# Kernel optimization log

Hardware: AMD Instinct MI355X
Metric: run time of the kernel (lower is better)

## Reference

```python
import jax, jax.numpy as jnp
import numpy as np
from itertools import product

C0, C1, C_IN, C_OUT = 16, 32, 1, 32
GRID = 768

def _enc(c):
    # injective int64 hash of 3D integer coords (values in [-4, 2043])
    return ((c[:, 0] + 4) * 2048 + (c[:, 1] + 4)) * 2048 + (c[:, 2] + 4)

def _build_km(coords, offsets):
    # kernel map for a stride-1 conv on one coordinate set:
    # per kernel offset o, pairs (in_idx, out_idx) with coords[in] == coords[out] + o
    N = coords.shape[0]
    keys = _enc(coords)
    order = np.argsort(keys)
    skeys = keys[order]
    ins, outs = [], []
    for o in offsets:
        qk = _enc(coords + np.asarray(o, np.int64))
        pos = np.searchsorted(skeys, qk)
        posc = np.clip(pos, 0, N - 1)
        valid = skeys[posc] == qk
        ins.append(order[posc[valid]].astype(np.int32))
        outs.append(np.nonzero(valid)[0].astype(np.int32))
    P = max(len(a) for a in ins)
    km_in = np.full((len(offsets), P), N, np.int32)   # pad -> zero row of x
    km_out = np.full((len(offsets), P), N, np.int32)  # pad -> dropped out row
    for k in range(len(offsets)):
        km_in[k, :len(ins[k])] = ins[k]
        km_out[k, :len(outs[k])] = outs[k]
    return km_in, km_out

def setup_inputs() -> dict:
    # voxelized surface heightfield: realistic sparse 3D point cloud occupancy
    xs, ys = np.meshgrid(np.arange(GRID), np.arange(GRID), indexing='ij')
    z = np.round(40.0 * np.sin(xs / 24.0) + 40.0 * np.cos(ys / 24.0)).astype(np.int64) + 128
    coords0 = np.stack([xs.ravel(), ys.ravel(), z.ravel()], 1).astype(np.int64)
    n0 = coords0.shape[0]
    offs27 = list(product((-1, 0, 1), repeat=3))
    km0_in, km0_out = _build_km(coords0, offs27)

    # stride-2 kernel-2 downsample: out coord = floor(c/2), offset = c mod 2
    u2 = coords0 // 2
    coords1, inv = np.unique(u2, axis=0, return_inverse=True)
    inv = inv.reshape(-1)
    n1 = coords1.shape[0]
    o = coords0 - 2 * u2
    kk = o[:, 0] * 4 + o[:, 1] * 2 + o[:, 2]
    ins, outs = [], []
    for k in range(8):
        m = np.nonzero(kk == k)[0]
        ins.append(m.astype(np.int32))
        outs.append(inv[m].astype(np.int32))
    P = max(len(a) for a in ins)
    kmd_in = np.full((8, P), n0, np.int32)
    kmd_out = np.full((8, P), n1, np.int32)
    for k in range(8):
        kmd_in[k, :len(ins[k])] = ins[k]
        kmd_out[k, :len(outs[k])] = outs[k]

    km1_in, km1_out = _build_km(coords1, offs27)

    key = jax.random.key(0)
    ks = jax.random.split(key, 6)
    w = lambda k, sh: jax.random.normal(k, sh, jnp.float32) * 0.1
    z32 = lambda c: jnp.zeros((c,), jnp.float32)
    return dict(
        in_feats=jnp.ones((n0, C_IN), jnp.float32),
        W_first=w(ks[0], (27, C_IN, C0)), b_first=z32(C0),
        W_pre=w(ks[1], (27, C0, C0)), b_pre=z32(C0),
        W_down=w(ks[2], (8, C0, C1)), b_down=z32(C1),
        W_r0=w(ks[3], (27, C1, C1)), b_r0=z32(C1),
        W_r1=w(ks[4], (27, C1, C1)), b_r1=z32(C1),
        W_fin=w(ks[5], (27, C1, C_OUT)), b_fin=z32(C_OUT),
        km0_in=jnp.asarray(km0_in), km0_out=jnp.asarray(km0_out),
        kmd_in=jnp.asarray(kmd_in), kmd_out=jnp.asarray(kmd_out),
        km1_in=jnp.asarray(km1_in), km1_out=jnp.asarray(km1_out),
        n1=int(n1),
    )

def _sparse_conv(x, W, b, km_in, km_out, n_out):
    # gather-GEMM-scatter sparse conv: out[j] += x[i] @ W[k] over pairs of offset k
    xp = jnp.concatenate([x, jnp.zeros((1, x.shape[1]), x.dtype)], 0)
    out = jnp.zeros((n_out + 1, W.shape[-1]), x.dtype)
    for k in range(W.shape[0]):  # static small loop over kernel offsets
        out = out.at[km_out[k]].add(xp[km_in[k]] @ W[k])
    return out[:n_out] + b

def reference(in_feats, W_first, b_first, W_pre, b_pre, W_down, b_down,
              W_r0, b_r0, W_r1, b_r1, W_fin, b_fin,
              km0_in, km0_out, kmd_in, kmd_out, km1_in, km1_out, n1):
    n0 = in_feats.shape[0]
    relu = jax.nn.relu
    # first_block: 3^3 conv + relu
    x = relu(_sparse_conv(in_feats, W_first, b_first, km0_in, km0_out, n0))
    cached = x  # cached_feature_list[0] (use_skip_connection=False)
    # blocks[0]: conv3x3 + relu, stride-2 downsample conv + relu
    x = relu(_sparse_conv(x, W_pre, b_pre, km0_in, km0_out, n0))
    x = relu(_sparse_conv(x, W_down, b_down, kmd_in, kmd_out, n1))
    # ResBlock
    r = relu(_sparse_conv(x, W_r0, b_r0, km1_in, km1_out, n1))
    r = _sparse_conv(r, W_r1, b_r1, km1_in, km1_out, n1)
    x = r + x
    # final conv (act=None)
    out = _sparse_conv(x, W_fin, b_fin, km1_in, km1_out, n1)
    return (out, cached)
```

## Files before the change

### kernel.cpp

```cpp
#include <hip/hip_runtime.h>


#define TPB 256
#define TPC 128

typedef __attribute__((ext_vector_type(8))) short short8;
typedef __attribute__((ext_vector_type(4))) float floatx4;

static __device__ __forceinline__ unsigned short f2b(float f) {
    union { float f; unsigned u; } v; v.f = f;
    unsigned r = v.u + 0x7fffu + ((v.u >> 16) & 1u);
    return (unsigned short)(r >> 16);
}
static __device__ __forceinline__ float b2f(unsigned short h) {
    union { unsigned u; float f; } v; v.u = ((unsigned)h) << 16;
    return v.f;
}

__global__ void scatter_tab(const int* __restrict__ km_in,
                            const int* __restrict__ km_out,
                            int* __restrict__ tab, long long rowcap, long long P,
                            long long total) {
    long long t = (long long)blockIdx.x * blockDim.x + threadIdx.x;
    if (t >= total) return;
    long long k = t / P;
    int o = km_out[t];
    tab[k * rowcap + o] = km_in[t];
}

__global__ void zero_pads(unsigned short* a, unsigned short* b, unsigned short* c,
                          unsigned short* d, unsigned short* e) {
    int t = threadIdx.x;
    if (t < 16) a[t] = 0;
    else if (t < 32) b[t - 16] = 0;
    else if (t < 64) c[t - 32] = 0;
    else if (t < 96) d[t - 64] = 0;
    else if (t < 128) e[t - 96] = 0;
}

__global__ void pack_w32(const float* __restrict__ W, unsigned short* __restrict__ Wp,
                         int K) {
    int t = blockIdx.x * blockDim.x + threadIdx.x;
    if (t >= K * 1024) return;
    int j = t & 7, n = (t >> 3) & 31, q = (t >> 8) & 3, k = t >> 10;
    Wp[t] = f2b(W[(k * 32 + q * 8 + j) * 32 + n]);
}

__global__ void pack_w16(const float* __restrict__ W, unsigned short* __restrict__ Wp,
                         int K2, int COUT, int Ksrc) {
    int t = blockIdx.x * blockDim.x + threadIdx.x;
    if (t >= K2 * 4 * COUT * 8) return;
    int j = t & 7;
    int r = t >> 3;
    int n = r % COUT; r /= COUT;
    int q = r & 3;
    int k2 = r >> 2;
    int ks = 2 * k2 + (q >> 1);
    int cin = (q & 1) * 8 + j;
    float v = (ks < Ksrc) ? W[(ks * 16 + cin) * COUT + n] : 0.f;
    Wp[t] = f2b(v);
}

__global__ __launch_bounds__(TPB) void conv_first_k(
    const float* __restrict__ xin, const float* __restrict__ W,
    const float* __restrict__ b, const int* __restrict__ tab, long long rowcap,
    int n0, float* __restrict__ outf, unsigned short* __restrict__ outb) {
    int j = blockIdx.x * blockDim.x + threadIdx.x;
    if (j >= n0) return;
    float acc[16];
#pragma unroll
    for (int c = 0; c < 16; ++c) acc[c] = b[c];
#pragma unroll
    for (int k = 0; k < 27; ++k) {
        int idx = tab[(long long)k * rowcap + j];
        bool ok = (unsigned)idx < (unsigned)n0;
        int cidx = ok ? idx : 0;
        float v = xin[cidx];
        v = ok ? v : 0.f;
        const float* Wk = W + k * 16;
#pragma unroll
        for (int c = 0; c < 16; ++c) acc[c] = fmaf(v, Wk[c], acc[c]);
    }
    float* orow = outf + (long long)j * 16;
    unsigned short* brow = outb + (long long)j * 16;
#pragma unroll
    for (int c = 0; c < 16; ++c) {
        float v = fmaxf(acc[c], 0.f);
        orow[c] = v;
        brow[c] = f2b(v);
    }
}

template <int CIN, int COUT, int STEPS, bool RELU, bool RES, bool WF32, bool WB16>
__global__ __launch_bounds__(TPC, 6) void conv_mfma(
    const unsigned short* __restrict__ xb,
    const unsigned short* __restrict__ Wp,
    const float* __restrict__ bias,
    const int* __restrict__ tab, long long rowcap, int n_in, int n_out,
    const unsigned short* __restrict__ resb,
    float* __restrict__ outf, unsigned short* __restrict__ outb) {
    constexpr int NT = COUT / 16;
    constexpr int CP = COUT + 4;
    __shared__ float red[64][CP];
    int w = (int)threadIdx.x >> 6;
    int lane = (int)threadIdx.x & 63;
    int m = lane & 15, q = lane >> 4;
    long long j0 = (long long)blockIdx.x * 64;

    floatx4 acc[4][NT];
#pragma unroll
    for (int t = 0; t < 4; ++t)
#pragma unroll
        for (int nt = 0; nt < NT; ++nt) acc[t][nt] = floatx4{0.f, 0.f, 0.f, 0.f};

    const int coff = (CIN == 32) ? q * 8 : (q & 1) * 8;
    constexpr int HSTEPS = (STEPS + 1) / 2;
#pragma unroll
    for (int i = 0; i < HSTEPS; ++i) {
        int s = 2 * i + w;
        if (s >= STEPS) break;
        int ks = (CIN == 32) ? s : 2 * s + (q >> 1);
        const int* trow = tab + (long long)ks * rowcap + j0 + m;
        int idx[4];
#pragma unroll
        for (int t = 0; t < 4; ++t) {
            unsigned v = (unsigned)trow[16 * t];
            idx[t] = (int)(v < (unsigned)n_in ? v : (unsigned)n_in);
        }
        short8 b0 = *(const short8*)(Wp + (((s * 4 + q) * COUT) + m) * 8);
        short8 b1;
        if (NT == 2) b1 = *(const short8*)(Wp + (((s * 4 + q) * COUT) + 16 + m) * 8);
#pragma unroll
        for (int t = 0; t < 4; ++t) {
            short8 a = *(const short8*)(xb + (long long)idx[t] * CIN + coff);
            acc[t][0] = __builtin_amdgcn_mfma_f32_16x16x32_bf16(a, b0, acc[t][0], 0, 0, 0);
            if (NT == 2)
                acc[t][1] = __builtin_amdgcn_mfma_f32_16x16x32_bf16(a, b1, acc[t][1], 0, 0, 0);
        }
    }

    if (w == 1) {
#pragma unroll
        for (int t = 0; t < 4; ++t)
#pragma unroll
            for (int u = 0; u < 4; ++u)
#pragma unroll
                for (int nt = 0; nt < NT; ++nt)
                    red[16 * t + 4 * q + u][16 * nt + m] = acc[t][nt][u];
    }
    __syncthreads();
    if (w == 1) return;

    float bs[2];
    bs[0] = bias[m];
    if (NT == 2) bs[1] = bias[16 + m];
#pragma unroll
    for (int t = 0; t < 4; ++t) {
#pragma unroll
        for (int u = 0; u < 4; ++u) {
            long long r = j0 + 16 * t + q * 4 + u;
            if (r < n_out) {
#pragma unroll
                for (int nt = 0; nt < NT; ++nt) {
                    float v = acc[t][nt][u] + red[16 * t + 4 * q + u][16 * nt + m] + bs[nt];
                    if (RES) v += b2f(resb[r * COUT + nt * 16 + m]);
                    if (RELU) v = fmaxf(v, 0.f);
                    if (WF32) outf[r * COUT + nt * 16 + m] = v;
                    if (WB16) outb[r * COUT + nt * 16 + m] = f2b(v);
                }
            }
        }
    }
}

static inline unsigned nblk(long long n, int b) { return (unsigned)((n + b - 1) / b); }
static inline size_t align64(size_t x) { return (x + 63) & ~(size_t)63; }

extern "C" void kernel_launch(void* const* d_in, const int* in_sizes, int n_in_cnt,
                              void* d_out, int out_size, void* d_ws, size_t ws_size,
                              hipStream_t stream) {
    const float* in_feats = (const float*)d_in[0];
    const float* W_first = (const float*)d_in[1];
    const float* b_first = (const float*)d_in[2];
    const float* W_pre   = (const float*)d_in[3];
    const float* b_pre   = (const float*)d_in[4];
    const float* W_down  = (const float*)d_in[5];
    const float* b_down  = (const float*)d_in[6];
    const float* W_r0    = (const float*)d_in[7];
    const float* b_r0    = (const float*)d_in[8];
    const float* W_r1    = (const float*)d_in[9];
    const float* b_r1    = (const float*)d_in[10];
    const float* W_fin   = (const float*)d_in[11];
    const float* b_fin   = (const float*)d_in[12];
    const int* km0_in  = (const int*)d_in[13];
    const int* km0_out = (const int*)d_in[14];
    const int* kmd_in  = (const int*)d_in[15];
    const int* kmd_out = (const int*)d_in[16];
    const int* km1_in  = (const int*)d_in[17];
    const int* km1_out = (const int*)d_in[18];

    const int n0 = in_sizes[0];
    const int n1 = (out_size - 16 * n0) / 32;
    const long long P0 = in_sizes[13] / 27;
    const long long Pd = in_sizes[15] / 8;
    const long long P1 = in_sizes[17] / 27;

    const long long rc0 = ((n0 + 64) / 64) * 64;
    const long long rc1 = ((n1 + 64) / 64) * 64;

    float* out_lo = (float*)d_out;
    float* cached = out_lo + (size_t)n1 * 32;

    char* base = (char*)d_ws;
    size_t off = 0;
    auto alloc = [&](size_t bytes) { void* p = base + off; off = align64(off + bytes); return p; };
    int* t0 = (int*)alloc(sizeof(int) * 28 * rc0);
    int* t1 = (int*)alloc(sizeof(int) * 27 * rc1);
    int* td = (int*)alloc(sizeof(int) * 8 * rc1);
    unsigned short* c0b   = (unsigned short*)alloc(sizeof(short) * 16 * (n0 + 1));
    unsigned short* x0pre = (unsigned short*)alloc(sizeof(short) * 16 * (n0 + 1));
    unsigned short* x1a   = (unsigned short*)alloc(sizeof(short) * 32 * (n1 + 1));
    unsigned short* x1b   = (unsigned short*)alloc(sizeof(short) * 32 * (n1 + 1));
    unsigned short* x1c   = (unsigned short*)alloc(sizeof(short) * 32 * (n1 + 1));
    unsigned short* wp_pre  = (unsigned short*)alloc(sizeof(short) * 14 * 4 * 16 * 8);
    unsigned short* wp_down = (unsigned short*)alloc(sizeof(short) * 4 * 4 * 32 * 8);
    unsigned short* wp_r0   = (unsigned short*)alloc(sizeof(short) * 27 * 1024);
    unsigned short* wp_r1   = (unsigned short*)alloc(sizeof(short) * 27 * 1024);
    unsigned short* wp_fin  = (unsigned short*)alloc(sizeof(short) * 27 * 1024);
    (void)ws_size; (void)n_in_cnt;

    scatter_tab<<<nblk(27 * P0, TPB), TPB, 0, stream>>>(km0_in, km0_out, t0, rc0, P0, 27 * P0);
    scatter_tab<<<nblk(27 * P1, TPB), TPB, 0, stream>>>(km1_in, km1_out, t1, rc1, P1, 27 * P1);
    scatter_tab<<<nblk(8 * Pd, TPB), TPB, 0, stream>>>(kmd_in, kmd_out, td, rc1, Pd, 8 * Pd);

    pack_w16<<<nblk(14 * 4 * 16 * 8, TPB), TPB, 0, stream>>>(W_pre, wp_pre, 14, 16, 27);
    pack_w16<<<nblk(4 * 4 * 32 * 8, TPB), TPB, 0, stream>>>(W_down, wp_down, 4, 32, 8);
    pack_w32<<<nblk(27 * 1024, TPB), TPB, 0, stream>>>(W_r0, wp_r0, 27);
    pack_w32<<<nblk(27 * 1024, TPB), TPB, 0, stream>>>(W_r1, wp_r1, 27);
    pack_w32<<<nblk(27 * 1024, TPB), TPB, 0, stream>>>(W_fin, wp_fin, 27);
    zero_pads<<<1, 160, 0, stream>>>(c0b + (size_t)n0 * 16, x0pre + (size_t)n0 * 16,
                                     x1a + (size_t)n1 * 32, x1b + (size_t)n1 * 32,
                                     x1c + (size_t)n1 * 32);

    conv_first_k<<<nblk(n0, TPB), TPB, 0, stream>>>(in_feats, W_first, b_first, t0, rc0,
                                                    n0, cached, c0b);
    const unsigned g0 = nblk(n0, 64), g1 = nblk(n1, 64);
    conv_mfma<16, 16, 14, true, false, false, true><<<g0, TPC, 0, stream>>>(
        c0b, wp_pre, b_pre, t0, rc0, n0, n0, nullptr, nullptr, x0pre);
    conv_mfma<16, 32, 4, true, false, false, true><<<g1, TPC, 0, stream>>>(
        x0pre, wp_down, b_down, td, rc1, n0, n1, nullptr, nullptr, x1a);
    conv_mfma<32, 32, 27, true, false, false, true><<<g1, TPC, 0, stream>>>(
        x1a, wp_r0, b_r0, t1, rc1, n1, n1, nullptr, nullptr, x1b);
    conv_mfma<32, 32, 27, false, true, false, true><<<g1, TPC, 0, stream>>>(
        x1b, wp_r1, b_r1, t1, rc1, n1, n1, x1a, nullptr, x1c);
    conv_mfma<32, 32, 27, false, false, true, false><<<g1, TPC, 0, stream>>>(
        x1c, wp_fin, b_fin, t1, rc1, n1, n1, nullptr, out_lo, nullptr);
}
```

Before: 527.7 us.

## Assign one 64-row tile per wave, drop LDS split-K reduction, fuse pack kernels

```diff
diff --git a/kernel.cpp b/kernel.cpp
--- a/kernel.cpp
+++ b/kernel.cpp
@@ -2,7 +2,6 @@
 
 
 #define TPB 256
-#define TPC 128
 
 typedef __attribute__((ext_vector_type(8))) short short8;
 typedef __attribute__((ext_vector_type(4))) float floatx4;
@@ -28,28 +27,9 @@
     tab[k * rowcap + o] = km_in[t];
 }
 
-__global__ void zero_pads(unsigned short* a, unsigned short* b, unsigned short* c,
-                          unsigned short* d, unsigned short* e) {
-    int t = threadIdx.x;
-    if (t < 16) a[t] = 0;
-    else if (t < 32) b[t - 16] = 0;
-    else if (t < 64) c[t - 32] = 0;
-    else if (t < 96) d[t - 64] = 0;
-    else if (t < 128) e[t - 96] = 0;
-}
-
-__global__ void pack_w32(const float* __restrict__ W, unsigned short* __restrict__ Wp,
-                         int K) {
-    int t = blockIdx.x * blockDim.x + threadIdx.x;
-    if (t >= K * 1024) return;
-    int j = t & 7, n = (t >> 3) & 31, q = (t >> 8) & 3, k = t >> 10;
-    Wp[t] = f2b(W[(k * 32 + q * 8 + j) * 32 + n]);
-}
-
-__global__ void pack_w16(const float* __restrict__ W, unsigned short* __restrict__ Wp,
-                         int K2, int COUT, int Ksrc) {
-    int t = blockIdx.x * blockDim.x + threadIdx.x;
-    if (t >= K2 * 4 * COUT * 8) return;
+static __device__ __forceinline__ void pack16_elem(
+    const float* __restrict__ W, unsigned short* __restrict__ Wp,
+    int t, int COUT, int Ksrc) {
     int j = t & 7;
     int r = t >> 3;
     int n = r % COUT; r /= COUT;
@@ -61,6 +41,41 @@
     Wp[t] = f2b(v);
 }
 
+__global__ void pack_all(const float* __restrict__ W_pre, const float* __restrict__ W_down,
+                         const float* __restrict__ W_r0, const float* __restrict__ W_r1,
+                         const float* __restrict__ W_fin,
+                         unsigned short* __restrict__ wp_pre, unsigned short* __restrict__ wp_down,
+                         unsigned short* __restrict__ wp_r0, unsigned short* __restrict__ wp_r1,
+                         unsigned short* __restrict__ wp_fin,
+                         unsigned short* p0, unsigned short* p1, unsigned short* p2,
+                         unsigned short* p3, unsigned short* p4) {
+    int t = blockIdx.x * blockDim.x + threadIdx.x;
+    if (t < 7168) { pack16_elem(W_pre, wp_pre, t, 16, 27); return; }
+    t -= 7168;
+    if (t < 4096) { pack16_elem(W_down, wp_down, t, 32, 8); return; }
+    t -= 4096;
+    if (t < 27648) {
+        int j = t & 7, n = (t >> 3) & 31, q = (t >> 8) & 3, k = t >> 10;
+        wp_r0[t] = f2b(W_r0[(k * 32 + q * 8 + j) * 32 + n]); return;
+    }
+    t -= 27648;
+    if (t < 27648) {
+        int j = t & 7, n = (t >> 3) & 31, q = (t >> 8) & 3, k = t >> 10;
+        wp_r1[t] = f2b(W_r1[(k * 32 + q * 8 + j) * 32 + n]); return;
+    }
+    t -= 27648;
+    if (t < 27648) {
+        int j = t & 7, n = (t >> 3) & 31, q = (t >> 8) & 3, k = t >> 10;
+        wp_fin[t] = f2b(W_fin[(k * 32 + q * 8 + j) * 32 + n]); return;
+    }
+    t -= 27648;
+    if (t < 16) p0[t] = 0;
+    else if (t < 32) p1[t - 16] = 0;
+    else if (t < 64) p2[t - 32] = 0;
+    else if (t < 96) p3[t - 64] = 0;
+    else if (t < 128) p4[t - 96] = 0;
+}
+
 __global__ __launch_bounds__(TPB) void conv_first_k(
     const float* __restrict__ xin, const float* __restrict__ W,
     const float* __restrict__ b, const int* __restrict__ tab, long long rowcap,
@@ -92,20 +107,22 @@
 }
 
 template <int CIN, int COUT, int STEPS, bool RELU, bool RES, bool WF32, bool WB16>
-__global__ __launch_bounds__(TPC, 6) void conv_mfma(
+__global__ __launch_bounds__(TPB, 4) void conv_mfma(
     const unsigned short* __restrict__ xb,
     const unsigned short* __restrict__ Wp,
     const float* __restrict__ bias,
     const int* __restrict__ tab, long long rowcap, int n_in, int n_out,
+    long long ntiles,
     const unsigned short* __restrict__ resb,
     float* __restrict__ outf, unsigned short* __restrict__ outb) {
     constexpr int NT = COUT / 16;
-    constexpr int CP = COUT + 4;
-    __shared__ float red[64][CP];
-    int w = (int)threadIdx.x >> 6;
+    int runs = (int)gridDim.x >> 3;
+    int sb = (int)(blockIdx.x & 7) * runs + (int)(blockIdx.x >> 3);
+    long long tile = (long long)sb * 4 + ((threadIdx.x >> 6) & 3);
+    if (tile >= ntiles) return;
     int lane = (int)threadIdx.x & 63;
     int m = lane & 15, q = lane >> 4;
-    long long j0 = (long long)blockIdx.x * 64;
+    long long j0 = tile * 64;
 
     floatx4 acc[4][NT];
 #pragma unroll
@@ -114,12 +131,9 @@
         for (int nt = 0; nt < NT; ++nt) acc[t][nt] = floatx4{0.f, 0.f, 0.f, 0.f};
 
     const int coff = (CIN == 32) ? q * 8 : (q & 1) * 8;
-    constexpr int HSTEPS = (STEPS + 1) / 2;
-#pragma unroll
-    for (int i = 0; i < HSTEPS; ++i) {
-        int s = 2 * i + w;
-        if (s >= STEPS) break;
-        int ks = (CIN == 32) ? s : 2 * s + (q >> 1);
+#pragma unroll
+    for (int s = 0; s < STEPS; ++s) {
+        const int ks = (CIN == 32) ? s : 2 * s + (q >> 1);
         const int* trow = tab + (long long)ks * rowcap + j0 + m;
         int idx[4];
 #pragma unroll
@@ -139,18 +153,6 @@
         }
     }
 
-    if (w == 1) {
-#pragma unroll
-        for (int t = 0; t < 4; ++t)
-#pragma unroll
-            for (int u = 0; u < 4; ++u)
-#pragma unroll
-                for (int nt = 0; nt < NT; ++nt)
-                    red[16 * t + 4 * q + u][16 * nt + m] = acc[t][nt][u];
-    }
-    __syncthreads();
-    if (w == 1) return;
-
     float bs[2];
     bs[0] = bias[m];
     if (NT == 2) bs[1] = bias[16 + m];
@@ -162,7 +164,7 @@
             if (r < n_out) {
 #pragma unroll
                 for (int nt = 0; nt < NT; ++nt) {
-                    float v = acc[t][nt][u] + red[16 * t + 4 * q + u][16 * nt + m] + bs[nt];
+                    float v = acc[t][nt][u] + bs[nt];
                     if (RES) v += b2f(resb[r * COUT + nt * 16 + m]);
                     if (RELU) v = fmaxf(v, 0.f);
                     if (WF32) outf[r * COUT + nt * 16 + m] = v;
@@ -174,6 +176,7 @@
 }
 
 static inline unsigned nblk(long long n, int b) { return (unsigned)((n + b - 1) / b); }
+static inline unsigned pad8(unsigned g) { return ((g + 7) / 8) * 8; }
 static inline size_t align64(size_t x) { return (x + 63) & ~(size_t)63; }
 
 extern "C" void kernel_launch(void* const* d_in, const int* in_sizes, int n_in_cnt,
@@ -207,6 +210,7 @@
 
     const long long rc0 = ((n0 + 64) / 64) * 64;
     const long long rc1 = ((n1 + 64) / 64) * 64;
+    const long long T0 = rc0 / 64, T1 = rc1 / 64;
 
     float* out_lo = (float*)d_out;
     float* cached = out_lo + (size_t)n1 * 32;
@@ -233,26 +237,24 @@
     scatter_tab<<<nblk(27 * P1, TPB), TPB, 0, stream>>>(km1_in, km1_out, t1, rc1, P1, 27 * P1);
     scatter_tab<<<nblk(8 * Pd, TPB), TPB, 0, stream>>>(kmd_in, kmd_out, td, rc1, Pd, 8 * Pd);
 
-    pack_w16<<<nblk(14 * 4 * 16 * 8, TPB), TPB, 0, stream>>>(W_pre, wp_pre, 14, 16, 27);
-    pack_w16<<<nblk(4 * 4 * 32 * 8, TPB), TPB, 0, stream>>>(W_down, wp_down, 4, 32, 8);
-    pack_w32<<<nblk(27 * 1024, TPB), TPB, 0, stream>>>(W_r0, wp_r0, 27);
-    pack_w32<<<nblk(27 * 1024, TPB), TPB, 0, stream>>>(W_r1, wp_r1, 27);
-    pack_w32<<<nblk(27 * 1024, TPB), TPB, 0, stream>>>(W_fin, wp_fin, 27);
-    zero_pads<<<1, 160, 0, stream>>>(c0b + (size_t)n0 * 16, x0pre + (size_t)n0 * 16,
-                                     x1a + (size_t)n1 * 32, x1b + (size_t)n1 * 32,
-                                     x1c + (size_t)n1 * 32);
+    const long long packN = 7168 + 4096 + 3 * 27648 + 128;
+    pack_all<<<nblk(packN, TPB), TPB, 0, stream>>>(
+        W_pre, W_down, W_r0, W_r1, W_fin,
+        wp_pre, wp_down, wp_r0, wp_r1, wp_fin,
+        c0b + (size_t)n0 * 16, x0pre + (size_t)n0 * 16,
+        x1a + (size_t)n1 * 32, x1b + (size_t)n1 * 32, x1c + (size_t)n1 * 32);
 
     conv_first_k<<<nblk(n0, TPB), TPB, 0, stream>>>(in_feats, W_first, b_first, t0, rc0,
                                                     n0, cached, c0b);
-    const unsigned g0 = nblk(n0, 64), g1 = nblk(n1, 64);
-    conv_mfma<16, 16, 14, true, false, false, true><<<g0, TPC, 0, stream>>>(
-        c0b, wp_pre, b_pre, t0, rc0, n0, n0, nullptr, nullptr, x0pre);
-    conv_mfma<16, 32, 4, true, false, false, true><<<g1, TPC, 0, stream>>>(
-        x0pre, wp_down, b_down, td, rc1, n0, n1, nullptr, nullptr, x1a);
-    conv_mfma<32, 32, 27, true, false, false, true><<<g1, TPC, 0, stream>>>(
-        x1a, wp_r0, b_r0, t1, rc1, n1, n1, nullptr, nullptr, x1b);
-    conv_mfma<32, 32, 27, false, true, false, true><<<g1, TPC, 0, stream>>>(
-        x1b, wp_r1, b_r1, t1, rc1, n1, n1, x1a, nullptr, x1c);
-    conv_mfma<32, 32, 27, false, false, true, false><<<g1, TPC, 0, stream>>>(
-        x1c, wp_fin, b_fin, t1, rc1, n1, n1, nullptr, out_lo, nullptr);
-}
+    const unsigned g0 = pad8(nblk(T0, 4)), g1 = pad8(nblk(T1, 4));
+    conv_mfma<16, 16, 14, true, false, false, true><<<g0, TPB, 0, stream>>>(
+        c0b, wp_pre, b_pre, t0, rc0, n0, n0, T0, nullptr, nullptr, x0pre);
+    conv_mfma<16, 32, 4, true, false, false, true><<<g1, TPB, 0, stream>>>(
+        x0pre, wp_down, b_down, td, rc1, n0, n1, T1, nullptr, nullptr, x1a);
+    conv_mfma<32, 32, 27, true, false, false, true><<<g1, TPB, 0, stream>>>(
+        x1a, wp_r0, b_r0, t1, rc1, n1, n1, T1, nullptr, nullptr, x1b);
+    conv_mfma<32, 32, 27, false, true, false, true><<<g1, TPB, 0, stream>>>(
+        x1b, wp_r1, b_r1, t1, rc1, n1, n1, T1, x1a, nullptr, x1c);
+    conv_mfma<32, 32, 27, false, false, true, false><<<g1, TPB, 0, stream>>>(
+        x1c, wp_fin, b_fin, t1, rc1, n1, n1, T1, nullptr, out_lo, nullptr);
+}
```

Result: faster. 494.9 us (-6.2%).
